# Kernel optimization log

Measured on AMD Instinct MI355X. Metric: run time of the kernel, lower is better.

The kernel has to match this reference:

```python
import jax, jax.numpy as jnp
import numpy as np

N_HEADS = 16
ROPE_THETA = 10000.0


def setup_inputs() -> dict:
    B, T, C = 4, 2048, 2048
    hd = C // N_HEADS  # 128
    key = jax.random.key(0)
    k1, k2, k3 = jax.random.split(key, 3)
    x = jax.random.normal(k1, (B, T, C), dtype=jnp.float32)
    # RoPE frequencies: angle[t, j] = t / theta^(2j/hd)
    inv_freq = 1.0 / (ROPE_THETA ** (jnp.arange(0, hd, 2, dtype=jnp.float32) / hd))  # (hd/2,)
    angles = jnp.arange(T, dtype=jnp.float32)[:, None] * inv_freq[None, :]  # (T, hd/2)
    freqs_cos = jnp.cos(angles)
    freqs_sin = jnp.sin(angles)
    W_qkv = jax.random.normal(k2, (C, 3 * C), dtype=jnp.float32) * (C ** -0.5)
    W_out = jax.random.normal(k3, (C, C), dtype=jnp.float32) * (C ** -0.5)
    return {"x": x, "freqs_cos": freqs_cos, "freqs_sin": freqs_sin, "W_qkv": W_qkv, "W_out": W_out}


def _apply_rope(t, cos, sin):
    # t: (B, H, T, hd); cos/sin: (T, hd/2). Interleaved-pair rotation, matching
    # torch view_as_complex on reshape(..., hd/2, 2).
    hd = t.shape[-1]
    tr = t.reshape(*t.shape[:-1], hd // 2, 2)
    x0, x1 = tr[..., 0], tr[..., 1]  # (B, H, T, hd/2)
    o0 = x0 * cos - x1 * sin
    o1 = x0 * sin + x1 * cos
    return jnp.stack([o0, o1], axis=-1).reshape(t.shape)


def reference(x, freqs_cos, freqs_sin, W_qkv, W_out):
    B, T, C = x.shape
    H = N_HEADS
    hd = C // H
    qkv = x @ W_qkv  # (B, T, 3C)
    q, k, v = jnp.split(qkv, 3, axis=-1)

    def heads(t):
        return t.reshape(B, T, H, hd).transpose(0, 2, 1, 3)  # (B, H, T, hd)

    cos, sin = freqs_cos[:T], freqs_sin[:T]
    q = _apply_rope(heads(q), cos, sin)
    k = _apply_rope(heads(k), cos, sin)
    v = heads(v)

    scale = hd ** -0.5
    scores = jnp.einsum('bhqd,bhkd->bhqk', q, k) * scale  # (B, H, T, T)
    causal = jnp.tril(jnp.ones((T, T), dtype=bool))
    scores = jnp.where(causal, scores, jnp.finfo(scores.dtype).min)
    attn = jax.nn.softmax(scores, axis=-1)
    out = jnp.einsum('bhqk,bhkd->bhqd', attn, v)  # (B, H, T, hd)
    out = out.transpose(0, 2, 1, 3).reshape(B, T, C)
    return out @ W_out, k, v
```

## Files before the change

### kernel.cpp

```cpp
#include <hip/hip_runtime.h>
#include <cstdint>
#include <cstddef>

typedef __attribute__((ext_vector_type(8))) short bf16x8;
typedef __attribute__((ext_vector_type(4))) float f32x4;

__device__ __forceinline__ unsigned short f2bf(float f) {
  union { float f; unsigned u; } v; v.f = f;
  unsigned r = v.u + 0x7FFFu + ((v.u >> 16) & 1u);
  return (unsigned short)(r >> 16);
}

#define GLL(gp, lp) __builtin_amdgcn_global_load_lds( \
    (const __attribute__((address_space(1))) void*)(gp), \
    (__attribute__((address_space(3))) void*)(lp), 16, 0, 0)

#define BARRIER() do { \
  __builtin_amdgcn_sched_barrier(0); \
  __builtin_amdgcn_s_barrier(); \
  __builtin_amdgcn_sched_barrier(0); } while (0)

#define WAIT_LGKM0() do { \
  asm volatile("s_waitcnt lgkmcnt(0)"); \
  __builtin_amdgcn_sched_barrier(0); } while (0)

#define WAIT_VM0() do { \
  asm volatile("s_waitcnt vmcnt(0)"); \
  __builtin_amdgcn_sched_barrier(0); } while (0)

__global__ void cvt_x_kernel(const float* __restrict__ x, unsigned short* __restrict__ xb, int n4) {
  int i = blockIdx.x * blockDim.x + threadIdx.x;
  if (i >= n4) return;
  const float4 v = reinterpret_cast<const float4*>(x)[i];
  ushort4 o;
  o.x = f2bf(v.x); o.y = f2bf(v.y); o.z = f2bf(v.z); o.w = f2bf(v.w);
  reinterpret_cast<ushort4*>(xb)[i] = o;
}

__global__ void transpose_kernel(const float* __restrict__ src, unsigned short* __restrict__ dst,
                                 int K, int N) {
  __shared__ float t[32][33];
  const int tx = threadIdx.x, ty = threadIdx.y;
  const int n0 = blockIdx.x * 32, k0 = blockIdx.y * 32;
#pragma unroll
  for (int i = 0; i < 4; ++i)
    t[ty + i * 8][tx] = src[(size_t)(k0 + ty + i * 8) * N + n0 + tx];
  __syncthreads();
#pragma unroll
  for (int i = 0; i < 4; ++i)
    dst[(size_t)(n0 + ty + i * 8) * K + k0 + tx] = f2bf(t[tx][ty + i * 8]);
}


template <int EPI>
__global__ void gemm2p_kernel(
    const unsigned short* __restrict__ Ag, const unsigned short* __restrict__ Bg,
    int K, int N, int mtMask, int mtShift,
    float* __restrict__ yout,
    const float* __restrict__ fcos, const float* __restrict__ fsin,
    unsigned short* __restrict__ q_ws, unsigned short* __restrict__ k_ws,
    unsigned short* __restrict__ vT_ws,
    float* __restrict__ k_out, float* __restrict__ v_out) {
  __shared__ unsigned short Asb[2][128 * 32];
  __shared__ unsigned short Bsb[2][128 * 32];

  const int tid = threadIdx.x;
  const int w = tid >> 6, lane = tid & 63;
  const int wr = w >> 1, wc = w & 1;
  const int g = lane >> 4, q16 = lane & 15;

  const int cpx = (int)gridDim.x >> 3;
  int bid = (int)blockIdx.x;
  bid = (bid & 7) * cpx + (bid >> 3);
  const int bm = bid & mtMask, bn = bid >> mtShift;
  const int m0 = bm << 7, n0 = bn << 7;
  const int NT = K >> 5;

  const int srow = lane >> 2;
  const int sslot = lane & 3;

  auto stageA = [&](int tile) {
    if (tile >= NT) return;
    unsigned short* dst = &Asb[tile & 1][0];
#pragma unroll
    for (int j = 0; j < 2; ++j) {
      const int row = w * 32 + j * 16 + srow;
      const int c = sslot ^ ((row >> 1) & 3);
      GLL(Ag + (size_t)(m0 + row) * K + tile * 32 + c * 8,
          dst + (w * 32 + j * 16) * 32);
    }
  };
  auto stageB = [&](int tile) {
    if (tile >= NT) return;
    unsigned short* dst = &Bsb[tile & 1][0];
#pragma unroll
    for (int j = 0; j < 2; ++j) {
      const int row = w * 32 + j * 16 + srow;
      const int c = sslot ^ ((row >> 1) & 3);
      GLL(Bg + (size_t)(n0 + row) * K + tile * 32 + c * 8,
          dst + (w * 32 + j * 16) * 32);
    }
  };

  f32x4 acc[4][4] = {};

  stageA(0); stageB(0);
  WAIT_VM0();
  BARRIER();

  for (int t = 0; t < NT; ++t) {
    stageA(t + 1); stageB(t + 1);
    const unsigned short* Ab = Asb[t & 1];
    const unsigned short* Bb = Bsb[t & 1];
    bf16x8 af[4], bfr[4];
#pragma unroll
    for (int i = 0; i < 4; ++i) {
      const int row = wr * 64 + i * 16 + q16;
      af[i] = *(const bf16x8*)(Ab + row * 32 + ((g ^ ((row >> 1) & 3)) << 3));
    }
#pragma unroll
    for (int j = 0; j < 4; ++j) {
      const int row = wc * 64 + j * 16 + q16;
      bfr[j] = *(const bf16x8*)(Bb + row * 32 + ((g ^ ((row >> 1) & 3)) << 3));
    }
    WAIT_LGKM0();
#pragma unroll
    for (int i = 0; i < 4; ++i)
#pragma unroll
      for (int j = 0; j < 4; ++j)
        acc[i][j] = __builtin_amdgcn_mfma_f32_16x16x32_bf16(af[i], bfr[j], acc[i][j], 0, 0, 0);
    WAIT_VM0();
    BARRIER();
  }

#pragma unroll
  for (int i = 0; i < 4; ++i) {
#pragma unroll
    for (int j = 0; j < 4; ++j) {
#pragma unroll
      for (int r = 0; r < 4; ++r) {
        const int m = m0 + wr * 64 + i * 16 + g * 4 + r;
        const int n = n0 + wc * 64 + j * 16 + q16;
        const float val = acc[i][j][r];
        if (EPI == 0) {
          yout[(size_t)m * N + n] = val;
        } else {
          const int region = bn >> 4;
          const int h = bn & 15;
          const int b = m >> 11, tt = m & 2047;
          const int dcol = n & 127;
          const size_t idx = ((size_t)((b * 16 + h) * 2048 + tt)) * 128 + dcol;
          if (region == 2) {
            v_out[idx] = val;
            vT_ws[((size_t)(b * 16 + h) * 128 + dcol) * 2048 + tt] = f2bf(val);
          } else {
            const int fi = dcol >> 1;
            const float c = fcos[tt * 64 + fi];
            const float s = fsin[tt * 64 + fi];
            const float part = __shfl_xor(val, 1);
            const float ro = (dcol & 1) ? (part * s + val * c) : (val * c - part * s);
            if (region == 0) {
              q_ws[idx] = f2bf(ro * 0.08838834764831845f);
            } else {
              k_out[idx] = ro;
              k_ws[idx] = f2bf(ro);
            }
          }
        }
      }
    }
  }
}

__global__ __launch_bounds__(256, 2) void attn_kernel(
    const unsigned short* __restrict__ q_ws,
    const unsigned short* __restrict__ k_ws,
    const unsigned short* __restrict__ vT_ws,
    unsigned short* __restrict__ attnout) {
  __shared__ unsigned short Kl[2][64 * 128];
  __shared__ unsigned short Vl[2][128 * 64];
  __shared__ unsigned short Pl[4][2][16 * 64];

  const int tid = threadIdx.x;
  const int w = tid >> 6, lane = tid & 63;
  const int g = lane >> 4, q16 = lane & 15;
  const int bh = blockIdx.x;
  const int qt = 15 - (int)blockIdx.y;
  const int b = bh >> 4, h = bh & 15;
  const int qbase = qt * 128;
  const int qb = qbase + w * 32;
  const size_t kvbase = (size_t)bh * 2048 * 128;

  const int krow_l = lane >> 4, kchunk = lane & 15;
  const int vrow_l = lane >> 3, vchunk = lane & 7;

  bf16x8 qf[2][4];
#pragma unroll
  for (int qs = 0; qs < 2; ++qs)
#pragma unroll
    for (int c = 0; c < 4; ++c)
      qf[qs][c] = *(const bf16x8*)&q_ws[kvbase + (size_t)(qb + qs * 16 + q16) * 128 + c * 32 + g * 8];

  f32x4 acc[2][8] = {};
  float mrun[2] = {-1e30f, -1e30f};
  float lrun[2] = {0.f, 0.f};

  const int nt = (qt + 1) * 2;

  auto stageK = [&](int buf, int kt) {
#pragma unroll
    for (int i = 0; i < 4; ++i) {
      const int slab = w * 4 + i;
      const int krow = slab * 4 + krow_l;
      GLL(k_ws + kvbase + (size_t)(kt + krow) * 128 + ((kchunk ^ (krow & 7)) << 3),
          ((unsigned short*)Kl[buf]) + slab * 512);
    }
  };
  auto stageV = [&](int buf, int kt) {
#pragma unroll
    for (int i = 0; i < 4; ++i) {
      const int slab = w * 4 + i;
      const int d = slab * 8 + vrow_l;
      GLL(vT_ws + kvbase + (size_t)d * 2048 + kt + ((vchunk ^ (d & 7)) << 3),
          ((unsigned short*)Vl[buf]) + slab * 512);
    }
  };

  stageK(0, 0); stageV(0, 0);
  int cur = 0;
  for (int it = 0; it < nt; ++it) {
    const int kt = it * 64;
    __syncthreads();
    if (it + 1 < nt) { stageK(cur ^ 1, kt + 64); stageV(cur ^ 1, kt + 64); }

    if (kt <= qb + 31) {
      f32x4 s[2][4];
#pragma unroll
      for (int qs = 0; qs < 2; ++qs)
#pragma unroll
        for (int t = 0; t < 4; ++t) s[qs][t] = f32x4{0.f, 0.f, 0.f, 0.f};
#pragma unroll
      for (int t = 0; t < 4; ++t) {
        const int key = t * 16 + q16;
#pragma unroll
        for (int c = 0; c < 4; ++c) {
          bf16x8 kf = *(const bf16x8*)&Kl[cur][key * 128 + (((c * 4 + g) ^ (key & 7)) << 3)];
          s[0][t] = __builtin_amdgcn_mfma_f32_16x16x32_bf16(kf, qf[0][c], s[0][t], 0, 0, 0);
          s[1][t] = __builtin_amdgcn_mfma_f32_16x16x32_bf16(kf, qf[1][c], s[1][t], 0, 0, 0);
        }
      }

#pragma unroll
      for (int qs = 0; qs < 2; ++qs) {
        const int qrow = qb + qs * 16 + q16;
        if (kt + 64 > qb + qs * 16) {
#pragma unroll
          for (int t = 0; t < 4; ++t)
#pragma unroll
            for (int r = 0; r < 4; ++r)
              if (kt + t * 16 + g * 4 + r > qrow) s[qs][t][r] = -1e30f;
        }
        float tm = s[qs][0][0];
#pragma unroll
        for (int t = 0; t < 4; ++t)
#pragma unroll
          for (int r = 0; r < 4; ++r) tm = fmaxf(tm, s[qs][t][r]);
        tm = fmaxf(tm, __shfl_xor(tm, 16));
        tm = fmaxf(tm, __shfl_xor(tm, 32));
        if (__any(tm > mrun[qs] + 8.0f)) {
          const float mnew = fmaxf(mrun[qs], tm);
          const float fac = __expf(mrun[qs] - mnew);
          lrun[qs] *= fac;
          mrun[qs] = mnew;
          float fr0 = __shfl(fac, g * 4 + 0), fr1 = __shfl(fac, g * 4 + 1);
          float fr2 = __shfl(fac, g * 4 + 2), fr3 = __shfl(fac, g * 4 + 3);
#pragma unroll
          for (int n = 0; n < 8; ++n) {
            acc[qs][n][0] *= fr0; acc[qs][n][1] *= fr1;
            acc[qs][n][2] *= fr2; acc[qs][n][3] *= fr3;
          }
        }
        float ps = 0.f;
        unsigned pk[8];
#pragma unroll
        for (int t = 0; t < 4; ++t) {
          const float p0 = __expf(s[qs][t][0] - mrun[qs]);
          const float p1 = __expf(s[qs][t][1] - mrun[qs]);
          const float p2 = __expf(s[qs][t][2] - mrun[qs]);
          const float p3 = __expf(s[qs][t][3] - mrun[qs]);
          ps += (p0 + p1) + (p2 + p3);
          pk[t * 2]     = (unsigned)f2bf(p0) | ((unsigned)f2bf(p1) << 16);
          pk[t * 2 + 1] = (unsigned)f2bf(p2) | ((unsigned)f2bf(p3) << 16);
        }
        ps += __shfl_xor(ps, 16);
        ps += __shfl_xor(ps, 32);
        lrun[qs] += ps;
#pragma unroll
        for (int t = 0; t < 4; ++t) {
          const unsigned byteoff = (unsigned)(q16 * 128) +
              (((unsigned)(t * 32 + g * 8)) ^ ((unsigned)(q16 & 7) << 4));
          *(uint2*)((char*)&Pl[w][qs][0] + byteoff) = make_uint2(pk[t * 2], pk[t * 2 + 1]);
        }
      }

      asm volatile("s_waitcnt lgkmcnt(0)" ::: "memory");
      __builtin_amdgcn_sched_barrier(0);
#pragma unroll
      for (int ks = 0; ks < 2; ++ks) {
        const unsigned pcol = ((unsigned)(ks * 64 + g * 16)) ^ ((unsigned)(q16 & 7) << 4);
        bf16x8 pa0 = *(const bf16x8*)((char*)&Pl[w][0][0] + q16 * 128 + pcol);
        bf16x8 pa1 = *(const bf16x8*)((char*)&Pl[w][1][0] + q16 * 128 + pcol);
#pragma unroll
        for (int n = 0; n < 8; ++n) {
          const int d = n * 16 + q16;
          bf16x8 vf = *(const bf16x8*)&Vl[cur][d * 64 + (((ks * 4 + g) ^ (d & 7)) << 3)];
          acc[0][n] = __builtin_amdgcn_mfma_f32_16x16x32_bf16(pa0, vf, acc[0][n], 0, 0, 0);
          acc[1][n] = __builtin_amdgcn_mfma_f32_16x16x32_bf16(pa1, vf, acc[1][n], 0, 0, 0);
        }
      }
    }
    cur ^= 1;
  }

#pragma unroll
  for (int qs = 0; qs < 2; ++qs) {
    float rl[4];
#pragma unroll
    for (int r = 0; r < 4; ++r) rl[r] = 1.0f / __shfl(lrun[qs], g * 4 + r);
#pragma unroll
    for (int n = 0; n < 8; ++n) {
#pragma unroll
      for (int r = 0; r < 4; ++r) {
        const int q = qb + qs * 16 + g * 4 + r;
        const int d = n * 16 + q16;
        attnout[((size_t)(b * 2048 + q)) * 2048 + h * 128 + d] = f2bf(acc[qs][n][r] * rl[r]);
      }
    }
  }
}

extern "C" void kernel_launch(void* const* d_in, const int* in_sizes, int n_in,
                              void* d_out, int out_size, void* d_ws, size_t ws_size,
                              hipStream_t stream) {
  (void)in_sizes; (void)n_in; (void)out_size; (void)ws_size;
  const float* x    = (const float*)d_in[0];
  const float* fcos = (const float*)d_in[1];
  const float* fsin = (const float*)d_in[2];
  const float* Wqkv = (const float*)d_in[3];
  const float* Wout = (const float*)d_in[4];

  float* out   = (float*)d_out;
  float* y_out = out;
  float* k_out = out + (size_t)16777216;
  float* v_out = out + (size_t)33554432;

  unsigned short* xb      = (unsigned short*)d_ws;
  unsigned short* wqkvT   = xb + 16777216;
  unsigned short* woutT   = wqkvT + 12582912;
  unsigned short* q_ws    = woutT + 4194304;
  unsigned short* k_ws    = q_ws + 16777216;
  unsigned short* vT_ws   = k_ws + 16777216;
  unsigned short* attnout = xb;

  cvt_x_kernel<<<16384, 256, 0, stream>>>(x, xb, 4194304);
  transpose_kernel<<<dim3(192, 64), dim3(32, 8), 0, stream>>>(Wqkv, wqkvT, 2048, 6144);
  transpose_kernel<<<dim3(64, 64), dim3(32, 8), 0, stream>>>(Wout, woutT, 2048, 2048);

  gemm2p_kernel<1><<<3072, 256, 0, stream>>>(
      xb, wqkvT, 2048, 6144, 63, 6,
      nullptr, fcos, fsin, q_ws, k_ws, vT_ws, k_out, v_out);

  attn_kernel<<<dim3(64, 16), 256, 0, stream>>>(q_ws, k_ws, vT_ws, attnout);

  gemm2p_kernel<0><<<1024, 256, 0, stream>>>(
      attnout, woutT, 2048, 2048, 63, 6,
      y_out, nullptr, nullptr, nullptr, nullptr, nullptr, nullptr, nullptr);
}
```

Before: 594.6 us.

## Triple-buffer GEMM LDS staging and remap blocks per XCD for locality

The GEMM kernel moves from double to triple-buffered LDS. Loads now run two tiles ahead, and a partial vmcnt wait replaces the full drain, so one barrier per iteration stays and global loads overlap the MFMA work. The block-to-tile mapping also changes so each XCD owns a contiguous group of eight M tiles across all N tiles, to improve L2 reuse of A rows. LDS use per block grows, which may lower occupancy.

```diff
diff --git a/kernel.cpp b/kernel.cpp
--- a/kernel.cpp
+++ b/kernel.cpp
@@ -24,8 +24,8 @@
   asm volatile("s_waitcnt lgkmcnt(0)"); \
   __builtin_amdgcn_sched_barrier(0); } while (0)
 
-#define WAIT_VM0() do { \
-  asm volatile("s_waitcnt vmcnt(0)"); \
+#define WAIT_VM(N) do { \
+  asm volatile("s_waitcnt vmcnt(" #N ")"); \
   __builtin_amdgcn_sched_barrier(0); } while (0)
 
 __global__ void cvt_x_kernel(const float* __restrict__ x, unsigned short* __restrict__ xb, int n4) {
@@ -55,24 +55,24 @@
 template <int EPI>
 __global__ void gemm2p_kernel(
     const unsigned short* __restrict__ Ag, const unsigned short* __restrict__ Bg,
-    int K, int N, int mtMask, int mtShift,
+    int K, int N,
     float* __restrict__ yout,
     const float* __restrict__ fcos, const float* __restrict__ fsin,
     unsigned short* __restrict__ q_ws, unsigned short* __restrict__ k_ws,
     unsigned short* __restrict__ vT_ws,
     float* __restrict__ k_out, float* __restrict__ v_out) {
-  __shared__ unsigned short Asb[2][128 * 32];
-  __shared__ unsigned short Bsb[2][128 * 32];
+  __shared__ unsigned short Asb[3][128 * 32];
+  __shared__ unsigned short Bsb[3][128 * 32];
 
   const int tid = threadIdx.x;
   const int w = tid >> 6, lane = tid & 63;
   const int wr = w >> 1, wc = w & 1;
   const int g = lane >> 4, q16 = lane & 15;
 
-  const int cpx = (int)gridDim.x >> 3;
-  int bid = (int)blockIdx.x;
-  bid = (bid & 7) * cpx + (bid >> 3);
-  const int bm = bid & mtMask, bn = bid >> mtShift;
+  const int xcd = (int)blockIdx.x & 7;
+  const int i = (int)blockIdx.x >> 3;
+  const int bm = xcd * 8 + (i & 7);
+  const int bn = i >> 3;
   const int m0 = bm << 7, n0 = bn << 7;
   const int NT = K >> 5;
 
@@ -81,7 +81,7 @@
 
   auto stageA = [&](int tile) {
     if (tile >= NT) return;
-    unsigned short* dst = &Asb[tile & 1][0];
+    unsigned short* dst = &Asb[tile % 3][0];
 #pragma unroll
     for (int j = 0; j < 2; ++j) {
       const int row = w * 32 + j * 16 + srow;
@@ -92,7 +92,7 @@
   };
   auto stageB = [&](int tile) {
     if (tile >= NT) return;
-    unsigned short* dst = &Bsb[tile & 1][0];
+    unsigned short* dst = &Bsb[tile % 3][0];
 #pragma unroll
     for (int j = 0; j < 2; ++j) {
       const int row = w * 32 + j * 16 + srow;
@@ -105,18 +105,20 @@
   f32x4 acc[4][4] = {};
 
   stageA(0); stageB(0);
-  WAIT_VM0();
-  BARRIER();
+  stageA(1); stageB(1);
 
   for (int t = 0; t < NT; ++t) {
-    stageA(t + 1); stageB(t + 1);
-    const unsigned short* Ab = Asb[t & 1];
-    const unsigned short* Bb = Bsb[t & 1];
+    if (t < NT - 1) { WAIT_VM(4); }
+    else            { WAIT_VM(0); }
+    BARRIER();
+    stageA(t + 2); stageB(t + 2);
+    const unsigned short* Ab = Asb[t % 3];
+    const unsigned short* Bb = Bsb[t % 3];
     bf16x8 af[4], bfr[4];
 #pragma unroll
-    for (int i = 0; i < 4; ++i) {
-      const int row = wr * 64 + i * 16 + q16;
-      af[i] = *(const bf16x8*)(Ab + row * 32 + ((g ^ ((row >> 1) & 3)) << 3));
+    for (int ii = 0; ii < 4; ++ii) {
+      const int row = wr * 64 + ii * 16 + q16;
+      af[ii] = *(const bf16x8*)(Ab + row * 32 + ((g ^ ((row >> 1) & 3)) << 3));
     }
 #pragma unroll
     for (int j = 0; j < 4; ++j) {
@@ -125,23 +127,21 @@
     }
     WAIT_LGKM0();
 #pragma unroll
-    for (int i = 0; i < 4; ++i)
+    for (int ii = 0; ii < 4; ++ii)
 #pragma unroll
       for (int j = 0; j < 4; ++j)
-        acc[i][j] = __builtin_amdgcn_mfma_f32_16x16x32_bf16(af[i], bfr[j], acc[i][j], 0, 0, 0);
-    WAIT_VM0();
-    BARRIER();
+        acc[ii][j] = __builtin_amdgcn_mfma_f32_16x16x32_bf16(af[ii], bfr[j], acc[ii][j], 0, 0, 0);
   }
 
 #pragma unroll
-  for (int i = 0; i < 4; ++i) {
+  for (int ii = 0; ii < 4; ++ii) {
 #pragma unroll
     for (int j = 0; j < 4; ++j) {
 #pragma unroll
       for (int r = 0; r < 4; ++r) {
-        const int m = m0 + wr * 64 + i * 16 + g * 4 + r;
+        const int m = m0 + wr * 64 + ii * 16 + g * 4 + r;
         const int n = n0 + wc * 64 + j * 16 + q16;
-        const float val = acc[i][j][r];
+        const float val = acc[ii][j][r];
         if (EPI == 0) {
           yout[(size_t)m * N + n] = val;
         } else {
@@ -367,12 +367,12 @@
   transpose_kernel<<<dim3(64, 64), dim3(32, 8), 0, stream>>>(Wout, woutT, 2048, 2048);
 
   gemm2p_kernel<1><<<3072, 256, 0, stream>>>(
-      xb, wqkvT, 2048, 6144, 63, 6,
+      xb, wqkvT, 2048, 6144,
       nullptr, fcos, fsin, q_ws, k_ws, vT_ws, k_out, v_out);
 
   attn_kernel<<<dim3(64, 16), 256, 0, stream>>>(q_ws, k_ws, vT_ws, attnout);
 
   gemm2p_kernel<0><<<1024, 256, 0, stream>>>(
-      attnout, woutT, 2048, 2048, 63, 6,
+      attnout, woutT, 2048, 2048,
       y_out, nullptr, nullptr, nullptr, nullptr, nullptr, nullptr, nullptr);
 }
```

After: 560.1 us. 1.06x faster.
